# Performance work log

Hardware: AMD Instinct MI355X
Metric: run time of the kernel (lower is better)

The kernel has to match this reference:

```python
import jax, jax.numpy as jnp
import numpy as np

B, S, D, H = 4, 1024, 1024, 16
HD = D // H  # head_dim = 64


def setup_inputs() -> dict:
    key = jax.random.key(0)
    ks = jax.random.split(key, 12)
    std = 1.0 / np.sqrt(D)
    inp = {
        "query": jax.random.normal(ks[0], (B, S, D), jnp.float32),
        "key": jax.random.normal(ks[1], (B, S, D), jnp.float32),
        "value": jax.random.normal(ks[2], (B, S, D), jnp.float32),
        # four Linear(embed_dim, embed_dim) layers: q, k, v, out
        "Wq": jax.random.normal(ks[3], (D, D), jnp.float32) * std,
        "bq": jnp.zeros((D,), jnp.float32),
        "Wk": jax.random.normal(ks[4], (D, D), jnp.float32) * std,
        "bk": jnp.zeros((D,), jnp.float32),
        "Wv": jax.random.normal(ks[5], (D, D), jnp.float32) * std,
        "bv": jnp.zeros((D,), jnp.float32),
        "Wo": jax.random.normal(ks[6], (D, D), jnp.float32) * std,
        "bo": jnp.zeros((D,), jnp.float32),
        # compressor: Linear(num_heads, 1)
        "Wc": jax.random.normal(ks[7], (H,), jnp.float32) / np.sqrt(H),
        "bc": jnp.zeros((), jnp.float32),
    }
    return inp


def reference(query, key, value, Wq, bq, Wk, bk, Wv, bv, Wo, bo, Wc, bc):
    b, s, d = query.shape
    h, hd = H, HD

    def proj(x, W, bias):
        # [b,s,d] @ [d,d] -> [b,h,s,hd]
        y = jnp.einsum('bsd,de->bse', x, W) + bias
        return y.reshape(b, s, h, hd).transpose(0, 2, 1, 3)

    q = proj(query, Wq, bq)
    k = proj(key, Wk, bk)
    v = proj(value, Wv, bv)

    scores = jnp.einsum('bhqd,bhkd->bhqk', q, k) / np.sqrt(hd)
    p_attn = jax.nn.softmax(scores, axis=-1)  # [b,h,s,s]; dropout is identity in eval

    x = jnp.einsum('bhqk,bhkd->bhqd', p_attn, v)
    x = x.transpose(0, 2, 1, 3).reshape(b, s, d)
    out = jnp.einsum('bsd,de->bse', x, Wo) + bo

    # head compression: Linear(num_heads, 1) over head axis -> [b,1,s,s]
    attn_c = (jnp.einsum('bhqk,h->bqk', p_attn, Wc) + bc)[:, None, :, :]
    return out, attn_c
```

## Files before the change

kernel.cpp:

```cpp
#include <hip/hip_runtime.h>
#include <hip/hip_bf16.h>

#define SS 1024
#define DD 1024
#define HH 16
#define HDh 64

typedef short bf16x8 __attribute__((ext_vector_type(8)));
typedef float f32x4 __attribute__((ext_vector_type(4)));

__device__ inline unsigned short f2bf(float f) {
    union { __hip_bfloat16 h; unsigned short u; } cv;
    cv.h = __float2bfloat16(f);
    return cv.u;
}
__device__ inline float bf2f(short u) {
    unsigned int x = ((unsigned int)(unsigned short)u) << 16;
    return __uint_as_float(x);
}

#define PIN4(a, b, c, d) asm volatile("" : "+v"(a), "+v"(b), "+v"(c), "+v"(d))

__device__ inline void gload_lds16(const unsigned short* g, unsigned short* l) {
    __builtin_amdgcn_global_load_lds(
        (const __attribute__((address_space(1))) unsigned int*)g,
        (__attribute__((address_space(3))) unsigned int*)l, 16, 0, 0);
}

__global__ __launch_bounds__(256) void prep(
    const float* __restrict__ a, const float* __restrict__ b, const float* __restrict__ c,
    unsigned short* __restrict__ oa, unsigned short* __restrict__ ob, unsigned short* __restrict__ oc,
    const float* __restrict__ Wq, const float* __restrict__ Wk,
    const float* __restrict__ Wv, const float* __restrict__ Wo,
    unsigned short* __restrict__ oq, unsigned short* __restrict__ okk,
    unsigned short* __restrict__ ov, unsigned short* __restrict__ oo)
{
    __shared__ float tile[32][33];
    int bid = blockIdx.x;
    if (bid < 4096) {
        size_t i = ((size_t)bid * 256 + threadIdx.x) * 4;
        float4 va = *(const float4*)(a + i);
        float4 vb = *(const float4*)(b + i);
        float4 vc = *(const float4*)(c + i);
        *(ushort4*)(oa + i) = make_ushort4(f2bf(va.x), f2bf(va.y), f2bf(va.z), f2bf(va.w));
        *(ushort4*)(ob + i) = make_ushort4(f2bf(vb.x), f2bf(vb.y), f2bf(vb.z), f2bf(vb.w));
        *(ushort4*)(oc + i) = make_ushort4(f2bf(vc.x), f2bf(vc.y), f2bf(vc.z), f2bf(vc.w));
    } else {
        int idx = bid - 4096;
        int z = idx >> 10;
        const float* W = z == 0 ? Wq : (z == 1 ? Wk : (z == 2 ? Wv : Wo));
        unsigned short* O = z == 0 ? oq : (z == 1 ? okk : (z == 2 ? ov : oo));
        int e0 = (idx & 31) * 32, d0 = ((idx >> 5) & 31) * 32;
        int r = threadIdx.x >> 3, c4 = (threadIdx.x & 7) * 4;
        float4 v = *(const float4*)(W + (size_t)(d0 + r) * DD + e0 + c4);
        tile[r][c4 + 0] = v.x; tile[r][c4 + 1] = v.y; tile[r][c4 + 2] = v.z; tile[r][c4 + 3] = v.w;
        __syncthreads();
        ushort4 u = make_ushort4(f2bf(tile[c4 + 0][r]), f2bf(tile[c4 + 1][r]),
                                 f2bf(tile[c4 + 2][r]), f2bf(tile[c4 + 3][r]));
        *(ushort4*)(O + (size_t)(e0 + r) * DD + d0 + c4) = u;
    }
}

__device__ inline void gemm128_core(const unsigned short* __restrict__ A,
                                    const unsigned short* __restrict__ Bt,
                                    const float* __restrict__ bias,
                                    void* __restrict__ out, int mode, float oscale,
                                    int m0, int n0)
{
    __shared__ unsigned short As[128 * 32];
    __shared__ unsigned short Bs[128 * 32];
    int t = threadIdx.x;
    int w = t >> 6, lane = t & 63, quad = lane >> 4, l15 = lane & 15;
    int wm = w >> 1, wn = w & 1;

    f32x4 zero = {0.f, 0.f, 0.f, 0.f};
    f32x4 acc[4][4];
#pragma unroll
    for (int i = 0; i < 4; i++)
#pragma unroll
        for (int j = 0; j < 4; j++) acc[i][j] = zero;

    for (int k0 = 0; k0 < DD; k0 += 32) {
        __syncthreads();
#pragma unroll
        for (int i = 0; i < 4; i++) {
            int chunk = w + i * 4;
            int half = chunk >> 3;
            int c = chunk & 7;
            const unsigned short* g = (half ? Bt : A)
                + (size_t)((half ? n0 : m0) + c * 16 + (lane >> 2)) * DD + k0 + (lane & 3) * 8;
            unsigned short* l = (half ? Bs : As) + c * 512 + lane * 8;
            gload_lds16(g, l);
        }
        __syncthreads();
        bf16x8 af[4], bfr[4];
#pragma unroll
        for (int mi = 0; mi < 4; mi++)
            af[mi] = *(const bf16x8*)&As[(wm * 64 + mi * 16 + l15) * 32 + quad * 8];
#pragma unroll
        for (int ni = 0; ni < 4; ni++)
            bfr[ni] = *(const bf16x8*)&Bs[(wn * 64 + ni * 16 + l15) * 32 + quad * 8];
#pragma unroll
        for (int mi = 0; mi < 4; mi++)
#pragma unroll
            for (int ni = 0; ni < 4; ni++)
                acc[mi][ni] = __builtin_amdgcn_mfma_f32_16x16x32_bf16(af[mi], bfr[ni], acc[mi][ni], 0, 0, 0);
    }

#pragma unroll
    for (int mi = 0; mi < 4; mi++)
#pragma unroll
        for (int ni = 0; ni < 4; ni++) {
            int n = n0 + wn * 64 + ni * 16 + l15;
            float bv = bias[n];
#pragma unroll
            for (int r = 0; r < 4; r++) {
                int m = m0 + wm * 64 + mi * 16 + quad * 4 + r;
                float v = (acc[mi][ni][r] + bv) * oscale;
                if (mode == 2) {
                    ((float*)out)[(size_t)m * DD + n] = v;
                } else {
                    int bb = m >> 10, s = m & 1023, hh = n >> 6, d = n & 63;
                    size_t head = (size_t)(bb * HH + hh) << 16;
                    size_t off;
                    if (mode == 0) {
                        off = head + (((size_t)(s >> 4) * 2 + (d >> 5)) * 64
                              + ((d >> 3) & 3) * 16 + (s & 15)) * 8 + (d & 7);
                    } else {
                        off = head + (((size_t)(s >> 5) * 4 + (d >> 4)) * 64
                              + ((s >> 3) & 3) * 16 + (d & 15)) * 8 + (s & 7);
                    }
                    ((unsigned short*)out)[off] = f2bf(v);
                }
            }
        }
}

#define SCLQ 0.18033688f

__global__ __launch_bounds__(256, 3) void gemm_qkv(
    const unsigned short* __restrict__ xq, const unsigned short* __restrict__ xk,
    const unsigned short* __restrict__ xv,
    const unsigned short* __restrict__ wtq, const unsigned short* __restrict__ wtk,
    const unsigned short* __restrict__ wtv,
    const float* __restrict__ bq, const float* __restrict__ bk, const float* __restrict__ bv,
    unsigned short* __restrict__ q, unsigned short* __restrict__ k, unsigned short* __restrict__ v)
{
    int bid = blockIdx.x;
    int swz = (bid & 7) * 96 + (bid >> 3);
    int z = swz >> 8, rem = swz & 255;
    int n0 = (rem & 7) * 128, m0 = (rem >> 3) * 128;
    const unsigned short* A  = z == 0 ? xq  : (z == 1 ? xk  : xv);
    const unsigned short* Bt = z == 0 ? wtq : (z == 1 ? wtk : wtv);
    const float* bias        = z == 0 ? bq  : (z == 1 ? bk  : bv);
    void* out                = z == 0 ? (void*)q : (z == 1 ? (void*)k : (void*)v);
    gemm128_core(A, Bt, bias, out, z == 2 ? 1 : 0, z == 0 ? SCLQ : 1.0f, m0, n0);
}

__global__ __launch_bounds__(256, 3) void gemm_o(
    const unsigned short* __restrict__ x, const unsigned short* __restrict__ wto,
    const float* __restrict__ bo, float* __restrict__ out)
{
    int bid = blockIdx.x;
    int swz = (bid & 7) * 32 + (bid >> 3);
    int n0 = (swz & 7) * 128, m0 = (swz >> 3) * 128;
    gemm128_core(x, wto, bo, out, 2, 1.0f, m0, n0);
}


__global__ __launch_bounds__(512, 4) void fattn_kernel(
    const unsigned short* __restrict__ qf, const unsigned short* __restrict__ kf,
    const unsigned short* __restrict__ vf, float* __restrict__ Z,
    unsigned short* __restrict__ xat)
{
    __shared__ __align__(16) unsigned short plds[8][640];
    int t = threadIdx.x, w = t >> 6, lane = t & 63, quad = lane >> 4, l15 = lane & 15;
    int bid = blockIdx.x;
    int swz = (bid & 7) * 64 + (bid >> 3);
    int bh = swz >> 3, m0 = (swz & 7) * 128;
    int b = bh >> 4, h = bh & 15;
    const unsigned short* qh = qf + ((size_t)bh << 16);
    const unsigned short* kh = kf + ((size_t)bh << 16);
    const unsigned short* vh = vf + ((size_t)bh << 16);

    bf16x8 qfrag[2];
    int s16b = (m0 >> 4) + w;
#pragma unroll
    for (int dh = 0; dh < 2; dh++)
        qfrag[dh] = *(const bf16x8*)(qh + (size_t)(s16b * 2 + dh) * 512 + lane * 8);

    f32x4 zero = {0.f, 0.f, 0.f, 0.f};
    f32x4 oacc[4];
#pragma unroll
    for (int ni = 0; ni < 4; ni++) oacc[ni] = zero;
    float zacc = 0.f;

    bf16x8 kc[4], vc[4];
#pragma unroll
    for (int i = 0; i < 4; i++) {
        kc[i] = *(const bf16x8*)(kh + (size_t)i * 512 + lane * 8);
        vc[i] = *(const bf16x8*)(vh + (size_t)i * 512 + lane * 8);
    }

    for (int kt = 0; kt < 32; kt++) {
        int nk = kt < 31 ? kt + 1 : 31;
        bf16x8 kn[4], vn[4];
#pragma unroll
        for (int i = 0; i < 4; i++) {
            kn[i] = *(const bf16x8*)(kh + ((size_t)nk * 4 + i) * 512 + lane * 8);
            vn[i] = *(const bf16x8*)(vh + ((size_t)nk * 4 + i) * 512 + lane * 8);
        }
        PIN4(kn[0], kn[1], kn[2], kn[3]);
        PIN4(vn[0], vn[1], vn[2], vn[3]);

        f32x4 st[2];
#pragma unroll
        for (int si = 0; si < 2; si++) {
            st[si] = __builtin_amdgcn_mfma_f32_16x16x32_bf16(kc[si * 2 + 0], qfrag[0], zero, 0, 0, 0);
            st[si] = __builtin_amdgcn_mfma_f32_16x16x32_bf16(kc[si * 2 + 1], qfrag[1], st[si], 0, 0, 0);
        }

#pragma unroll
        for (int si = 0; si < 2; si++) {
            float p0 = exp2f(st[si][0]);
            float p1 = exp2f(st[si][1]);
            float p2 = exp2f(st[si][2]);
            float p3 = exp2f(st[si][3]);
            zacc += (p0 + p1) + (p2 + p3);
            unsigned int pk0 = (unsigned int)f2bf(p0) | ((unsigned int)f2bf(p1) << 16);
            unsigned int pk1 = (unsigned int)f2bf(p2) | ((unsigned int)f2bf(p3) << 16);
            *(uint2*)&plds[w][l15 * 40 + si * 16 + quad * 4] = make_uint2(pk0, pk1);
        }
        bf16x8 pa = *(const bf16x8*)&plds[w][l15 * 40 + quad * 8];

#pragma unroll
        for (int ni = 0; ni < 4; ni++)
            oacc[ni] = __builtin_amdgcn_mfma_f32_16x16x32_bf16(pa, vc[ni], oacc[ni], 0, 0, 0);

#pragma unroll
        for (int i = 0; i < 4; i++) { kc[i] = kn[i]; vc[i] = vn[i]; }
    }

    float zt = zacc;
    zt += __shfl_xor(zt, 16);
    zt += __shfl_xor(zt, 32);
    if (quad == 0)
        Z[(size_t)bh * 1024 + m0 + w * 16 + l15] = zt;

#pragma unroll
    for (int r = 0; r < 4; r++) {
        int qrow = quad * 4 + r;
        float iz = 1.f / __shfl(zt, qrow);
        int q = m0 + w * 16 + qrow;
#pragma unroll
        for (int ni = 0; ni < 4; ni++)
            xat[((size_t)(b * 1024 + q)) * 1024 + h * 64 + ni * 16 + l15] =
                f2bf(oacc[ni][r] * iz);
    }
}

__global__ __launch_bounds__(256, 3) void tail_kernel(
    const unsigned short* __restrict__ qf, const unsigned short* __restrict__ kf,
    const float* __restrict__ Z, const float* __restrict__ Wc,
    const float* __restrict__ bcp, float* __restrict__ attc,
    const unsigned short* __restrict__ xat, const unsigned short* __restrict__ wto,
    const float* __restrict__ bo, float* __restrict__ out0)
{
    if (blockIdx.x >= 512) {
        int bid2 = blockIdx.x - 512;
        int swz = (bid2 & 7) * 32 + (bid2 >> 3);
        int n0 = (swz & 7) * 128, m0 = (swz >> 3) * 128;
        gemm128_core(xat, wto, bo, out0, 2, 1.0f, m0, n0);
        return;
    }
    __shared__ unsigned short ks[2][8192];
    int t = threadIdx.x, w = t >> 6, lane = t & 63, quad = lane >> 4, l15 = lane & 15;
    int bid = blockIdx.x;
    int u = (bid & 7) * 64 + (bid >> 3);
    int kb = u & 7, qg = (u >> 3) & 15, b = u >> 7;
    int qt = qg * 4 + w;
    int q = qt * 16 + l15;
    float bc = *bcp;
    f32x4 zero = {0.f, 0.f, 0.f, 0.f};
    f32x4 acc[4][2];
#pragma unroll
    for (int kt = 0; kt < 4; kt++)
#pragma unroll
        for (int si = 0; si < 2; si++) acc[kt][si] = zero;

    float wzv[16];
#pragma unroll
    for (int h = 0; h < 16; h++)
        wzv[h] = Wc[h] / Z[(size_t)(b * 16 + h) * 1024 + q];

    {
        const unsigned short* src = kf + ((size_t)(b * 16) << 16) + (size_t)(kb * 16) * 512;
#pragma unroll
        for (int i = 0; i < 4; i++) {
            int c = w + i * 4;
            gload_lds16(src + (size_t)c * 512 + lane * 8, ks[0] + c * 512 + lane * 8);
        }
    }
    __syncthreads();

    int cb = 0;
    for (int h = 0; h < 16; h++) {
        int bh = b * 16 + h;
        const unsigned short* qh = qf + ((size_t)bh << 16);
        bf16x8 qfr0 = *(const bf16x8*)(qh + (size_t)(qt * 2 + 0) * 512 + lane * 8);
        bf16x8 qfr1 = *(const bf16x8*)(qh + (size_t)(qt * 2 + 1) * 512 + lane * 8);
        if (h < 15) {
            const unsigned short* src = kf + ((size_t)(bh + 1) << 16) + (size_t)(kb * 16) * 512;
#pragma unroll
            for (int i = 0; i < 4; i++) {
                int c = w + i * 4;
                gload_lds16(src + (size_t)c * 512 + lane * 8, ks[cb ^ 1] + c * 512 + lane * 8);
            }
        }
        float wz = wzv[h];
#pragma unroll
        for (int kt = 0; kt < 4; kt++) {
            bf16x8 kfr[4];
#pragma unroll
            for (int i = 0; i < 4; i++)
                kfr[i] = *(const bf16x8*)&ks[cb][(size_t)(kt * 4 + i) * 512 + lane * 8];
#pragma unroll
            for (int si = 0; si < 2; si++) {
                f32x4 st = __builtin_amdgcn_mfma_f32_16x16x32_bf16(kfr[si * 2 + 0], qfr0, zero, 0, 0, 0);
                st = __builtin_amdgcn_mfma_f32_16x16x32_bf16(kfr[si * 2 + 1], qfr1, st, 0, 0, 0);
#pragma unroll
                for (int r = 0; r < 4; r++)
                    acc[kt][si][r] += wz * exp2f(st[r]);
            }
        }
        __syncthreads();
        cb ^= 1;
    }
#pragma unroll
    for (int kt = 0; kt < 4; kt++)
#pragma unroll
        for (int si = 0; si < 2; si++) {
            float4 vv = make_float4(acc[kt][si][0] + bc, acc[kt][si][1] + bc,
                                    acc[kt][si][2] + bc, acc[kt][si][3] + bc);
            *(float4*)(attc + ((size_t)(b * 1024 + q)) * 1024 + kb * 128 + kt * 32 + si * 16 + quad * 4) = vv;
        }
}

#define LDK(f) (*(const bf16x8*)(kh + ((size_t)(f) * 64 + lane) * 8))
#define LDV(f) (*(const bf16x8*)(vh + ((size_t)(f) * 64 + lane) * 8))

__global__ __launch_bounds__(1024, 4) void attn_kernel(
    const unsigned short* __restrict__ qf, const unsigned short* __restrict__ kf,
    const unsigned short* __restrict__ vf, const float* __restrict__ Wc,
    const float* __restrict__ bcp, unsigned short* __restrict__ xout,
    float* __restrict__ attc)
{
    __shared__ float accc[16][1028];
    __shared__ unsigned short tsc[16][16][36];

    int t = threadIdx.x, w = t >> 6, lane = t & 63, quad = lane >> 4, l15 = lane & 15;
    int b = blockIdx.x >> 6, qt = blockIdx.x & 63;
    int h = w;

    for (int i = t; i < 16 * 1028; i += 1024) (&accc[0][0])[i] = 0.f;
    __syncthreads();

    const unsigned short* qh = qf + ((size_t)(b * HH + h) << 16);
    const unsigned short* kh = kf + ((size_t)(b * HH + h) << 16);
    const unsigned short* vh = vf + ((size_t)(b * HH + h) << 16);
    float wc = Wc[h], bc = *bcp;
    f32x4 zero = {0.f, 0.f, 0.f, 0.f};

    bf16x8 a0 = *(const bf16x8*)(qh + ((size_t)(qt * 2 + 0) * 64 + lane) * 8);
    bf16x8 a1 = *(const bf16x8*)(qh + ((size_t)(qt * 2 + 1) * 64 + lane) * 8);

    float rs[4] = {0.f, 0.f, 0.f, 0.f};
    bf16x8 c0 = LDK(0), c1 = LDK(1), c2 = LDK(2), c3 = LDK(3);
    PIN4(c0, c1, c2, c3);
    bf16x8 d0 = LDK(4), d1 = LDK(5), d2 = LDK(6), d3 = LDK(7);
    PIN4(d0, d1, d2, d3);
#pragma unroll 2
    for (int g = 0; g < 32; g++) {
        int gn = g < 30 ? g + 2 : 31;
        bf16x8 n0 = LDK(gn * 4 + 0), n1 = LDK(gn * 4 + 1);
        bf16x8 n2 = LDK(gn * 4 + 2), n3 = LDK(gn * 4 + 3);
        PIN4(n0, n1, n2, n3);
        f32x4 s0 = zero, s1 = zero;
        s0 = __builtin_amdgcn_mfma_f32_16x16x32_bf16(a0, c0, s0, 0, 0, 0);
        s0 = __builtin_amdgcn_mfma_f32_16x16x32_bf16(a1, c1, s0, 0, 0, 0);
        s1 = __builtin_amdgcn_mfma_f32_16x16x32_bf16(a0, c2, s1, 0, 0, 0);
        s1 = __builtin_amdgcn_mfma_f32_16x16x32_bf16(a1, c3, s1, 0, 0, 0);
#pragma unroll
        for (int r = 0; r < 4; r++) rs[r] += exp2f(s0[r]) + exp2f(s1[r]);
        c0 = d0; c1 = d1; c2 = d2; c3 = d3;
        d0 = n0; d1 = n1; d2 = n2; d3 = n3;
    }
#pragma unroll
    for (int r = 0; r < 4; r++) {
        rs[r] += __shfl_xor(rs[r], 1);
        rs[r] += __shfl_xor(rs[r], 2);
        rs[r] += __shfl_xor(rs[r], 4);
        rs[r] += __shfl_xor(rs[r], 8);
    }
    float invC[4], sC[4];
#pragma unroll
    for (int r = 0; r < 4; r++) { invC[r] = 1.f / rs[r]; sC[r] = wc * invC[r]; }

    f32x4 o0 = zero, o1 = zero, o2 = zero, o3 = zero;
    int cc0 = (2 * w) & 31;
    bf16x8 k0 = LDK(cc0 * 4 + 0), k1 = LDK(cc0 * 4 + 1);
    bf16x8 k2 = LDK(cc0 * 4 + 2), k3 = LDK(cc0 * 4 + 3);
    PIN4(k0, k1, k2, k3);
    bf16x8 v0 = LDV(cc0 * 4 + 0), v1 = LDV(cc0 * 4 + 1);
    bf16x8 v2 = LDV(cc0 * 4 + 2), v3 = LDV(cc0 * 4 + 3);
    PIN4(v0, v1, v2, v3);
#pragma unroll 2
    for (int i = 0; i < 32; i++) {
        int cc = (i + 2 * w) & 31;
        int cn = ((i + 1) + 2 * w) & 31;
        bf16x8 kn0 = LDK(cn * 4 + 0), kn1 = LDK(cn * 4 + 1);
        bf16x8 kn2 = LDK(cn * 4 + 2), kn3 = LDK(cn * 4 + 3);
        PIN4(kn0, kn1, kn2, kn3);
        bf16x8 vn0 = LDV(cn * 4 + 0), vn1 = LDV(cn * 4 + 1);
        bf16x8 vn2 = LDV(cn * 4 + 2), vn3 = LDV(cn * 4 + 3);
        PIN4(vn0, vn1, vn2, vn3);

        f32x4 s0 = zero, s1 = zero;
        s0 = __builtin_amdgcn_mfma_f32_16x16x32_bf16(a0, k0, s0, 0, 0, 0);
        s0 = __builtin_amdgcn_mfma_f32_16x16x32_bf16(a1, k1, s0, 0, 0, 0);
        s1 = __builtin_amdgcn_mfma_f32_16x16x32_bf16(a0, k2, s1, 0, 0, 0);
        s1 = __builtin_amdgcn_mfma_f32_16x16x32_bf16(a1, k3, s1, 0, 0, 0);

#pragma unroll
        for (int r = 0; r < 4; r++) {
            float p0 = exp2f(s0[r]);
            float p1 = exp2f(s1[r]);
            int row = quad * 4 + r;
            tsc[w][row][l15] = f2bf(p0);
            tsc[w][row][16 + l15] = f2bf(p1);
            atomicAdd(&accc[row][cc * 32 + l15], sC[r] * p0);
            atomicAdd(&accc[row][cc * 32 + 16 + l15], sC[r] * p1);
        }
        bf16x8 ap = *(const bf16x8*)&tsc[w][l15][quad * 8];

        o0 = __builtin_amdgcn_mfma_f32_16x16x32_bf16(ap, v0, o0, 0, 0, 0);
        o1 = __builtin_amdgcn_mfma_f32_16x16x32_bf16(ap, v1, o1, 0, 0, 0);
        o2 = __builtin_amdgcn_mfma_f32_16x16x32_bf16(ap, v2, o2, 0, 0, 0);
        o3 = __builtin_amdgcn_mfma_f32_16x16x32_bf16(ap, v3, o3, 0, 0, 0);
        k0 = kn0; k1 = kn1; k2 = kn2; k3 = kn3;
        v0 = vn0; v1 = vn1; v2 = vn2; v3 = vn3;
    }

    f32x4 oo[4] = {o0, o1, o2, o3};
#pragma unroll
    for (int j = 0; j < 4; j++)
#pragma unroll
        for (int r = 0; r < 4; r++) {
            int row = quad * 4 + r;
            xout[((size_t)(b * SS) + qt * 16 + row) * DD + h * 64 + j * 16 + l15] =
                f2bf(oo[j][r] * invC[r]);
        }

    __syncthreads();
    for (int i = t; i < 16 * 1024; i += 1024) {
        int row = i >> 10, col = i & 1023;
        attc[((size_t)b * SS + qt * 16 + row) * SS + col] = accc[row][col] + bc;
    }
}

extern "C" void kernel_launch(void* const* d_in, const int* in_sizes, int n_in,
                              void* d_out, int out_size, void* d_ws, size_t ws_size,
                              hipStream_t stream) {
    const float* query = (const float*)d_in[0];
    const float* key   = (const float*)d_in[1];
    const float* value = (const float*)d_in[2];
    const float* Wq = (const float*)d_in[3];
    const float* bq = (const float*)d_in[4];
    const float* Wk = (const float*)d_in[5];
    const float* bk = (const float*)d_in[6];
    const float* Wv = (const float*)d_in[7];
    const float* bv = (const float*)d_in[8];
    const float* Wo = (const float*)d_in[9];
    const float* bo = (const float*)d_in[10];
    const float* Wc = (const float*)d_in[11];
    const float* bc = (const float*)d_in[12];

    unsigned short* ws  = (unsigned short*)d_ws;
    unsigned short* xq  = ws;
    unsigned short* xk  = xq  + (size_t)4194304;
    unsigned short* xv  = xk  + (size_t)4194304;
    unsigned short* wtq = xv  + (size_t)4194304;
    unsigned short* wtk = wtq + (size_t)1048576;
    unsigned short* wtv = wtk + (size_t)1048576;
    unsigned short* wto = wtv + (size_t)1048576;
    unsigned short* qfb = wto + (size_t)1048576;
    unsigned short* kfb = qfb + (size_t)4194304;
    unsigned short* vfb = kfb + (size_t)4194304;
    unsigned short* xat = vfb + (size_t)4194304;

    float* out0 = (float*)d_out;
    float* attc = out0 + (size_t)4194304;

    const size_t base_bytes = 67108864;
    const size_t z_bytes = 262144;
    bool fast = ws_size >= base_bytes + z_bytes;

    hipLaunchKernelGGL(prep, dim3(8192), dim3(256), 0, stream,
                       query, key, value, xq, xk, xv,
                       Wq, Wk, Wv, Wo, wtq, wtk, wtv, wto);
    hipLaunchKernelGGL(gemm_qkv, dim3(768), dim3(256), 0, stream,
                       xq, xk, xv, wtq, wtk, wtv, bq, bk, bv, qfb, kfb, vfb);

    if (fast) {
        float* Zbuf = (float*)((char*)d_ws + base_bytes);
        hipLaunchKernelGGL(fattn_kernel, dim3(512), dim3(512), 0, stream,
                           qfb, kfb, vfb, Zbuf, xat);
        hipLaunchKernelGGL(tail_kernel, dim3(768), dim3(256), 0, stream,
                           qfb, kfb, Zbuf, Wc, bc, attc,
                           xat, wto, bo, out0);
    } else {
        hipLaunchKernelGGL(attn_kernel, dim3(256), dim3(1024), 0, stream,
                           qfb, kfb, vfb, Wc, bc, xat, attc);
        hipLaunchKernelGGL(gemm_o, dim3(256), dim3(256), 0, stream,
                           xat, wto, bo, out0);
    }
}
```

Measured before the change: 239.3 us.

## Stage attention K/V tiles through LDS and deepen GEMM k-step to 64

The shared GEMM core now loads 64-wide K slices per iteration (double the LDS tiles) and runs two MFMA sub-steps per barrier pair, halving the number of synchronizations. The flash attention kernel stops having every wave independently load K/V fragments from global memory with register prefetch. Instead, the 8 waves cooperatively load each K/V tile into LDS once via global_load_lds and then read fragments from LDS. This cuts redundant global/L2 traffic but adds two barriers per tile and drops the register-level prefetch overlap.

Measured after the change: 246.2 us. +2.9%, slower.

```diff
diff --git a/kernel.cpp b/kernel.cpp
--- a/kernel.cpp
+++ b/kernel.cpp
@@ -67,8 +67,8 @@
                                     void* __restrict__ out, int mode, float oscale,
                                     int m0, int n0)
 {
-    __shared__ unsigned short As[128 * 32];
-    __shared__ unsigned short Bs[128 * 32];
+    __shared__ unsigned short As[128 * 64];
+    __shared__ unsigned short Bs[128 * 64];
     int t = threadIdx.x;
     int w = t >> 6, lane = t & 63, quad = lane >> 4, l15 = lane & 15;
     int wm = w >> 1, wn = w & 1;
@@ -80,31 +80,35 @@
 #pragma unroll
         for (int j = 0; j < 4; j++) acc[i][j] = zero;
 
-    for (int k0 = 0; k0 < DD; k0 += 32) {
+    for (int k0 = 0; k0 < DD; k0 += 64) {
         __syncthreads();
 #pragma unroll
-        for (int i = 0; i < 4; i++) {
+        for (int i = 0; i < 8; i++) {
             int chunk = w + i * 4;
-            int half = chunk >> 3;
-            int c = chunk & 7;
+            int half = chunk >> 4;
+            int sub = chunk & 15;
             const unsigned short* g = (half ? Bt : A)
-                + (size_t)((half ? n0 : m0) + c * 16 + (lane >> 2)) * DD + k0 + (lane & 3) * 8;
-            unsigned short* l = (half ? Bs : As) + c * 512 + lane * 8;
+                + (size_t)((half ? n0 : m0) + (sub >> 1) * 16 + (lane >> 2)) * DD
+                + k0 + (sub & 1) * 32 + (lane & 3) * 8;
+            unsigned short* l = (half ? Bs : As) + sub * 512 + lane * 8;
             gload_lds16(g, l);
         }
         __syncthreads();
-        bf16x8 af[4], bfr[4];
-#pragma unroll
-        for (int mi = 0; mi < 4; mi++)
-            af[mi] = *(const bf16x8*)&As[(wm * 64 + mi * 16 + l15) * 32 + quad * 8];
-#pragma unroll
-        for (int ni = 0; ni < 4; ni++)
-            bfr[ni] = *(const bf16x8*)&Bs[(wn * 64 + ni * 16 + l15) * 32 + quad * 8];
-#pragma unroll
-        for (int mi = 0; mi < 4; mi++)
+#pragma unroll
+        for (int kk = 0; kk < 2; kk++) {
+            bf16x8 af[4], bfr[4];
+#pragma unroll
+            for (int mi = 0; mi < 4; mi++)
+                af[mi] = *(const bf16x8*)&As[((wm * 4 + mi) * 2 + kk) * 512 + l15 * 32 + quad * 8];
 #pragma unroll
             for (int ni = 0; ni < 4; ni++)
-                acc[mi][ni] = __builtin_amdgcn_mfma_f32_16x16x32_bf16(af[mi], bfr[ni], acc[mi][ni], 0, 0, 0);
+                bfr[ni] = *(const bf16x8*)&Bs[((wn * 4 + ni) * 2 + kk) * 512 + l15 * 32 + quad * 8];
+#pragma unroll
+            for (int mi = 0; mi < 4; mi++)
+#pragma unroll
+                for (int ni = 0; ni < 4; ni++)
+                    acc[mi][ni] = __builtin_amdgcn_mfma_f32_16x16x32_bf16(af[mi], bfr[ni], acc[mi][ni], 0, 0, 0);
+        }
     }
 
 #pragma unroll
@@ -173,6 +177,8 @@
     const unsigned short* __restrict__ vf, float* __restrict__ Z,
     unsigned short* __restrict__ xat)
 {
+    __shared__ __align__(16) unsigned short kls[2048];
+    __shared__ __align__(16) unsigned short vls[2048];
     __shared__ __align__(16) unsigned short plds[8][640];
     int t = threadIdx.x, w = t >> 6, lane = t & 63, quad = lane >> 4, l15 = lane & 15;
     int bid = blockIdx.x;
@@ -195,23 +201,21 @@
     for (int ni = 0; ni < 4; ni++) oacc[ni] = zero;
     float zacc = 0.f;
 
-    bf16x8 kc[4], vc[4];
-#pragma unroll
-    for (int i = 0; i < 4; i++) {
-        kc[i] = *(const bf16x8*)(kh + (size_t)i * 512 + lane * 8);
-        vc[i] = *(const bf16x8*)(vh + (size_t)i * 512 + lane * 8);
-    }
+    const unsigned short* ssrc = (w < 4 ? kh + (size_t)w * 512
+                                        : vh + (size_t)(w - 4) * 512) + lane * 8;
+    unsigned short* sdst = (w < 4 ? kls + w * 512 : vls + (w - 4) * 512) + lane * 8;
 
     for (int kt = 0; kt < 32; kt++) {
-        int nk = kt < 31 ? kt + 1 : 31;
-        bf16x8 kn[4], vn[4];
+        __syncthreads();
+        gload_lds16(ssrc + (size_t)kt * 2048, sdst);
+        __syncthreads();
+
+        bf16x8 kc[4], vc[4];
 #pragma unroll
         for (int i = 0; i < 4; i++) {
-            kn[i] = *(const bf16x8*)(kh + ((size_t)nk * 4 + i) * 512 + lane * 8);
-            vn[i] = *(const bf16x8*)(vh + ((size_t)nk * 4 + i) * 512 + lane * 8);
-        }
-        PIN4(kn[0], kn[1], kn[2], kn[3]);
-        PIN4(vn[0], vn[1], vn[2], vn[3]);
+            kc[i] = *(const bf16x8*)&kls[i * 512 + lane * 8];
+            vc[i] = *(const bf16x8*)&vls[i * 512 + lane * 8];
+        }
 
         f32x4 st[2];
 #pragma unroll
@@ -236,9 +240,6 @@
 #pragma unroll
         for (int ni = 0; ni < 4; ni++)
             oacc[ni] = __builtin_amdgcn_mfma_f32_16x16x32_bf16(pa, vc[ni], oacc[ni], 0, 0, 0);
-
-#pragma unroll
-        for (int i = 0; i < 4; i++) { kc[i] = kn[i]; vc[i] = vn[i]; }
     }
 
     float zt = zacc;
```
